# Kernel tuning notes

Hardware: AMD Instinct MI355X
Metric: run time of the kernel (lower is better)

## Reference

```python
import jax, jax.numpy as jnp
import numpy as np

B, S, D, H, HD = 2, 4096, 768, 12, 64
W = 256           # one-sided window (attention_window=512)
C = S // W        # number of query chunks
NEG = -1e9


def _heads(x):
    # [B,S,D] -> [B,H,S,HD]
    return x.reshape(B, S, H, HD).transpose(0, 2, 1, 3)


def setup_inputs() -> dict:
    key = jax.random.key(0)
    ks = jax.random.split(key, 9)
    sc = 0.02
    w = lambda i: jax.random.normal(ks[i], (D, D), jnp.float32) * sc
    return {
        "hidden_states": jax.random.normal(ks[0], (B, S, D), jnp.float32),
        "Wq": w(1), "Wk": w(2), "Wv": w(3),
        "Wqg": w(4), "Wkg": w(5), "Wvg": w(6),
        "Wo": w(7),
        "attention_mask": jnp.ones((B, S), jnp.int32),
    }


def reference(hidden_states, Wq, Wk, Wv, Wqg, Wkg, Wvg, Wo, attention_mask):
    x = hidden_states
    scale = 1.0 / float(np.sqrt(HD))
    q = _heads(x @ Wq) * scale           # [B,H,S,HD]
    k = _heads(x @ Wk)
    v = _heads(x @ Wv)

    # ---- banded sliding-window attention (chunked, no [S,S] matrix) ----
    idx = jnp.arange(C)[:, None] * W + jnp.arange(3 * W)[None, :]   # [C,3W] into padded seq
    key_pos = idx - W                                               # absolute key position
    kp = jnp.pad(k, ((0, 0), (0, 0), (W, W), (0, 0)))
    vp = jnp.pad(v, ((0, 0), (0, 0), (W, W), (0, 0)))
    kc = kp[:, :, idx]                   # [B,H,C,3W,HD]
    vc = vp[:, :, idx]
    qc = q.reshape(B, H, C, W, HD)
    band = jnp.einsum('bhcqd,bhckd->bhcqk', qc, kc)  # [B,H,C,W,3W]

    qi = jnp.arange(W)[:, None]
    kj = jnp.arange(3 * W)[None, :]
    diag_ok = (kj >= qi) & (kj <= qi + 2 * W)              # |i-j| <= W
    valid = (key_pos >= 0) & (key_pos < S) & (key_pos != 0)  # in-range, dedupe global key 0
    mask = diag_ok[None, :, :] & valid[:, None, :]          # [C,W,3W]
    band = jnp.where(mask[None, None], band, NEG)

    # padding mask on keys
    m = jnp.where(attention_mask > 0, 0.0, NEG).astype(jnp.float32)  # [B,S]
    mp = jnp.pad(m, ((0, 0), (W, W)), constant_values=NEG)
    band = band + mp[:, idx][:, None, :, None, :]
    band = band.reshape(B, H, S, 3 * W)

    # every local query also attends to the global (CLS, pos 0) key
    gsc = jnp.einsum('bhsd,bhgd->bhsg', q, k[:, :, 0:1])   # [B,H,S,1]
    gsc = gsc + m[:, 0][:, None, None, None]

    scores = jnp.concatenate([gsc, band], axis=-1)          # [B,H,S,1+3W]
    probs = jax.nn.softmax(scores, axis=-1)
    pg = probs[..., :1]                                     # global-key prob
    pb = probs[..., 1:].reshape(B, H, C, W, 3 * W)
    out = jnp.einsum('bhcqk,bhckd->bhcqd', pb, vc).reshape(B, H, S, HD)
    out = out + pg * v[:, :, 0:1]

    # ---- global query (CLS) full attention with dedicated projections ----
    qg = _heads(x @ Wqg)[:, :, 0:1] * scale                 # [B,H,1,HD]
    kg = _heads(x @ Wkg)
    vg = _heads(x @ Wvg)
    gs = jnp.einsum('bhgd,bhsd->bhgs', qg, kg) + m[:, None, None, :]
    og = jnp.einsum('bhgs,bhsd->bhgd', jax.nn.softmax(gs, axis=-1), vg)
    out = out.at[:, :, 0:1].set(og)

    out = out.transpose(0, 2, 1, 3).reshape(B, S, D) @ Wo
    return out
```

## Files before the change

kernel.cpp:

```cpp
#include <hip/hip_runtime.h>

#define S_LEN 4096
#define NH 12
#define HDIM 64
#define DMODEL 768
#define NEGF -1.0e9f
#define TOK0_SPLITS 16

typedef __attribute__((ext_vector_type(8))) short bf16x8;
typedef __attribute__((ext_vector_type(4))) float f32x4;

__device__ __forceinline__ short f2b(float f) {
  union { float f; unsigned u; } v; v.f = f;
  unsigned r = v.u + 0x7fffu + ((v.u >> 16) & 1u);
  return (short)(r >> 16);
}
__device__ __forceinline__ float b2f(short s) {
  union { unsigned u; float f; } v; v.u = ((unsigned)(unsigned short)s) << 16;
  return v.f;
}

__global__ __launch_bounds__(256) void k_pre(const float* __restrict__ x,
                                             const float* __restrict__ Wq,
                                             const float* __restrict__ Wk,
                                             const float* __restrict__ Wv,
                                             const float* __restrict__ Wkg,
                                             const float* __restrict__ Wvg,
                                             const float* __restrict__ Wo,
                                             const float* __restrict__ Wqg,
                                             const int* __restrict__ amask,
                                             short* __restrict__ xb,
                                             short* __restrict__ W5t,
                                             short* __restrict__ Wot,
                                             float* __restrict__ qg,
                                             float* __restrict__ mvb) {
  __shared__ float smem[1056];
  int bid = blockIdx.x, tid = threadIdx.x;
  if (bid < 6144) {
    int i = bid * 256 + tid;
    float4 v = ((const float4*)x)[i];
    ((short4*)xb)[i] = make_short4(f2b(v.x), f2b(v.y), f2b(v.z), f2b(v.w));
  } else if (bid < 9600) {
    int zb = bid - 6144;
    int z = zb / 576, rem = zb - z * 576;
    int by = rem / 24, bx = rem - by * 24;
    const float* src; float scale = 1.f; short* dst;
    switch (z) {
      case 0: src = Wq;  scale = 0.125f * 1.44269504f; dst = W5t; break;
      case 1: src = Wk;  dst = W5t + 589824; break;
      case 2: src = Wv;  dst = W5t + 2 * 589824; break;
      case 3: src = Wkg; dst = W5t + 3 * 589824; break;
      case 4: src = Wvg; dst = W5t + 4 * 589824; break;
      default: src = Wo; dst = Wot; break;
    }
    int tx = tid & 31, ty = tid >> 5;
    int kb = by * 32, nb = bx * 32;
    for (int i = 0; i < 4; i++) smem[(ty + 8 * i) * 33 + tx] = src[(kb + ty + 8 * i) * 768 + nb + tx];
    __syncthreads();
    for (int i = 0; i < 4; i++)
      dst[(nb + ty + 8 * i) * 768 + kb + tx] = f2b(smem[tx * 33 + ty + 8 * i] * scale);
  } else if (bid < 9632) {
    int zb = bid - 9600;
    int b = zb >> 4, s = (zb & 15) * 256 + tid;
    mvb[b * S_LEN + s] = (s != 0 && amask[b * S_LEN + s] > 0) ? 0.f : NEGF;
  } else {
    int zb = bid - 9632;
    int h = zb % 12, b = zb / 12;
    int out = tid & 63, slice = tid >> 6;
    float* xr = smem;
    float* ps = smem + 768;
    for (int i = tid; i < 768; i += 256) xr[i] = x[(long)b * S_LEN * 768 + i];
    __syncthreads();
    float a = 0.f;
    int n = h * 64 + out;
#pragma unroll 8
    for (int k = slice * 192; k < slice * 192 + 192; k++) a += xr[k] * Wqg[k * 768 + n];
    ps[slice * 64 + out] = a;
    __syncthreads();
    if (tid < 64)
      qg[b * 768 + h * 64 + tid] = (ps[tid] + ps[64 + tid] + ps[128 + tid] + ps[192 + tid]) * 0.125f;
  }
}

__global__ __launch_bounds__(256) void k_gemm(const short* __restrict__ A,
                                              const short* __restrict__ Bt, int K, int mode,
                                              short* __restrict__ qkv, float* __restrict__ outf) {
  __shared__ short Al[2][128 * 32];
  __shared__ short Bl[2][128 * 32];
  int bid = blockIdx.x;
  int xcd = bid & 7, ii = bid >> 3;
  int bm = xcd * 8 + (ii & 7), bn = ii >> 3;
  int tid = threadIdx.x;
  int bm0 = bm * 128, bn0 = bn * 128;
  int w = tid >> 6, lane = tid & 63, g = lane >> 4, r16 = lane & 15;
  int wr = (w >> 1) * 64, wc = (w & 1) * 64;
  f32x4 zero4 = {0.f, 0.f, 0.f, 0.f};
  f32x4 acc[4][4];
  for (int m = 0; m < 4; m++) for (int n = 0; n < 4; n++) acc[m][n] = zero4;
  int srow = w * 32 + (lane >> 2);
  int scol = (lane & 3) * 8;
#define G_STAGE(BUF, KT)                                                              \
  do {                                                                                \
    for (int i = 0; i < 2; i++) {                                                     \
      const short* ga = &A[(long)(bm0 + srow + i * 16) * K + (KT) + scol];            \
      const short* gb = &Bt[(long)(bn0 + srow + i * 16) * K + (KT) + scol];           \
      __builtin_amdgcn_global_load_lds(                                               \
          (const __attribute__((address_space(1))) void*)ga,                          \
          (__attribute__((address_space(3))) void*)&Al[BUF][(w * 32 + i * 16) * 32],  \
          16, 0, 0);                                                                  \
      __builtin_amdgcn_global_load_lds(                                               \
          (const __attribute__((address_space(1))) void*)gb,                          \
          (__attribute__((address_space(3))) void*)&Bl[BUF][(w * 32 + i * 16) * 32],  \
          16, 0, 0);                                                                  \
    }                                                                                 \
  } while (0)
  int nt = K >> 5;
  G_STAGE(0, 0);
  __syncthreads();
  int cur = 0;
  for (int t = 0; t < nt; t++) {
    if (t + 1 < nt) G_STAGE(cur ^ 1, (t + 1) * 32);
    bf16x8 af[4], bfv[4];
    for (int m = 0; m < 4; m++) af[m] = *(const bf16x8*)&Al[cur][(wr + m * 16 + r16) * 32 + g * 8];
    for (int n = 0; n < 4; n++) bfv[n] = *(const bf16x8*)&Bl[cur][(wc + n * 16 + r16) * 32 + g * 8];
    for (int m = 0; m < 4; m++)
      for (int n = 0; n < 4; n++)
        acc[m][n] = __builtin_amdgcn_mfma_f32_16x16x32_bf16(af[m], bfv[n], acc[m][n], 0, 0, 0);
    __syncthreads();
    cur ^= 1;
  }
#undef G_STAGE
  for (int m = 0; m < 4; m++)
    for (int n = 0; n < 4; n++)
      for (int reg = 0; reg < 4; reg++) {
        int row = bm0 + wr + m * 16 + g * 4 + reg;
        int col = bn0 + wc + n * 16 + r16;
        float val = acc[m][n][reg];
        if (mode == 0) {
          int proj = col / 768;
          int rem = col - proj * 768;
          int hh = rem >> 6, d = rem & 63;
          int bb = row >> 12, s = row & 4095;
          qkv[(long)proj * 6291456 + ((((long)bb * NH + hh) * S_LEN + s) << 6) + d] = f2b(val);
        } else {
          outf[(long)row * 768 + col] = val;
        }
      }
}

__global__ __launch_bounds__(256) void k_vt(const short* __restrict__ V, short* __restrict__ Vt) {
  __shared__ short buf[64][72];
  int st = blockIdx.x, bh = blockIdx.y;
  int tid = threadIdx.x;
  long base = (long)bh * S_LEN * HDIM;
  int s0 = st * 64;
  int r = tid >> 2, c = (tid & 3) * 16;
  *(int4*)&buf[r][c]     = *(const int4*)&V[base + (long)(s0 + r) * HDIM + c];
  *(int4*)&buf[r][c + 8] = *(const int4*)&V[base + (long)(s0 + r) * HDIM + c + 8];
  __syncthreads();
  int d = tid >> 2, sc = (tid & 3) * 16;
  short tmp[16];
#pragma unroll
  for (int j = 0; j < 16; j++) tmp[j] = buf[sc + j][d];
  long ob = base + (long)d * S_LEN + s0 + sc;
  *(int4*)&Vt[ob]     = *(const int4*)&tmp[0];
  *(int4*)&Vt[ob + 8] = *(const int4*)&tmp[8];
}

#define PSTRIDE 68

__device__ __forceinline__ void band_chunk(
    int ks0, int qrow0, int g, int r16,
    const bf16x8 (&qf)[2][2], const bf16x8 (&kf)[4][2], const bf16x8 (&vf)[4][2],
    const float (&mv)[4],
    float (&mstate)[2][4], float (&lstate)[2][4], f32x4 (&acc)[2][4],
    short* Plds) {
  int dlo = ks0 - qrow0;
  bool fullok = (dlo >= -224) && (dlo <= 192);
  for (int m = 0; m < 2; m++) {
    f32x4 s[4];
    f32x4 zero4 = {0.f, 0.f, 0.f, 0.f};
    for (int n = 0; n < 4; n++) {
      f32x4 z = __builtin_amdgcn_mfma_f32_16x16x32_bf16(qf[m][0], kf[n][0], zero4, 0, 0, 0);
      s[n] = __builtin_amdgcn_mfma_f32_16x16x32_bf16(qf[m][1], kf[n][1], z, 0, 0, 0);
    }
    float p[4][4], rmax[4];
    for (int reg = 0; reg < 4; reg++) rmax[reg] = NEGF;
    if (fullok) {
      for (int n = 0; n < 4; n++)
        for (int reg = 0; reg < 4; reg++) {
          float val = s[n][reg] + mv[n];
          p[n][reg] = val;
          rmax[reg] = fmaxf(rmax[reg], val);
        }
    } else {
      int qbase = qrow0 + m * 16 + g * 4;
      for (int n = 0; n < 4; n++) {
        int kpos = ks0 + n * 16 + r16;
        for (int reg = 0; reg < 4; reg++) {
          int qpos = qbase + reg;
          bool ok = (kpos >= qpos - 256) && (kpos <= qpos + 256);
          float val = ok ? (s[n][reg] + mv[n]) : NEGF;
          p[n][reg] = val;
          rmax[reg] = fmaxf(rmax[reg], val);
        }
      }
    }
    for (int reg = 0; reg < 4; reg++) {
      float r = rmax[reg];
      r = fmaxf(r, __shfl_xor(r, 1));
      r = fmaxf(r, __shfl_xor(r, 2));
      r = fmaxf(r, __shfl_xor(r, 4));
      r = fmaxf(r, __shfl_xor(r, 8));
      rmax[reg] = r;
    }
    bool over = false;
    for (int reg = 0; reg < 4; reg++) over = over || (rmax[reg] > mstate[m][reg] + 8.f);
    if (__any((int)over)) {
      float scal[4];
      for (int reg = 0; reg < 4; reg++) {
        float mn = fmaxf(mstate[m][reg], rmax[reg]);
        scal[reg] = __builtin_amdgcn_exp2f(mstate[m][reg] - mn);
        mstate[m][reg] = mn;
      }
      float rs[4] = {0.f, 0.f, 0.f, 0.f};
      for (int n = 0; n < 4; n++)
        for (int reg = 0; reg < 4; reg++) {
          float e = __builtin_amdgcn_exp2f(p[n][reg] - mstate[m][reg]);
          p[n][reg] = e;
          rs[reg] += e;
        }
      for (int reg = 0; reg < 4; reg++) {
        float r = rs[reg];
        r += __shfl_xor(r, 1);
        r += __shfl_xor(r, 2);
        r += __shfl_xor(r, 4);
        r += __shfl_xor(r, 8);
        lstate[m][reg] = lstate[m][reg] * scal[reg] + r;
      }
      for (int n = 0; n < 4; n++)
        for (int reg = 0; reg < 4; reg++) acc[m][n][reg] *= scal[reg];
    } else {
      float rs[4] = {0.f, 0.f, 0.f, 0.f};
      for (int n = 0; n < 4; n++)
        for (int reg = 0; reg < 4; reg++) {
          float e = __builtin_amdgcn_exp2f(p[n][reg] - mstate[m][reg]);
          p[n][reg] = e;
          rs[reg] += e;
        }
      for (int reg = 0; reg < 4; reg++) {
        float r = rs[reg];
        r += __shfl_xor(r, 1);
        r += __shfl_xor(r, 2);
        r += __shfl_xor(r, 4);
        r += __shfl_xor(r, 8);
        lstate[m][reg] += r;
      }
    }
    for (int n = 0; n < 4; n++)
      for (int reg = 0; reg < 4; reg++)
        Plds[(g * 4 + reg) * PSTRIDE + n * 16 + r16] = f2b(p[n][reg]);
    bf16x8 pa[2];
    for (int ks = 0; ks < 2; ks++)
      pa[ks] = *(const bf16x8*)&Plds[r16 * PSTRIDE + ks * 32 + g * 8];
    for (int n = 0; n < 4; n++)
      for (int ks = 0; ks < 2; ks++)
        acc[m][n] = __builtin_amdgcn_mfma_f32_16x16x32_bf16(pa[ks], vf[n][ks], acc[m][n], 0, 0, 0);
  }
}

__global__ __launch_bounds__(256, 2) void k_attn(const short* __restrict__ Qb,
                                                 const short* __restrict__ Kb,
                                                 const short* __restrict__ Vb,
                                                 const short* __restrict__ Vtb,
                                                 const short* __restrict__ Kg,
                                                 const short* __restrict__ Vg,
                                                 const float* __restrict__ qg,
                                                 const int* __restrict__ amask,
                                                 const float* __restrict__ mvb,
                                                 short* __restrict__ oattn,
                                                 float* __restrict__ part) {
  __shared__ short Plds[4][16 * PSTRIDE];
  __shared__ float mrg[2][48][65];
  __shared__ float fsm[592];
  int bid = blockIdx.x, tid = threadIdx.x;
  if (bid < 1536) {
    int qt = bid & 63, rest = bid >> 6;
    int h = rest % NH, b = rest / NH;
    int w = tid >> 6, lane = tid & 63, g = lane >> 4, r16 = lane & 15;
    int pair = w >> 1;
    int par = w & 1;
    long bhof = ((long)(b * NH + h)) * S_LEN * HDIM;
    int qrow0 = qt * 64 + pair * 32;

    bf16x8 qf[2][2];
    for (int m = 0; m < 2; m++)
      for (int ks = 0; ks < 2; ks++)
        qf[m][ks] = *(const bf16x8*)&Qb[bhof + (long)(qrow0 + m * 16 + r16) * HDIM + ks * 32 + g * 8];

    float mstate[2][4], lstate[2][4];
    f32x4 acc[2][4];
    if (par == 0) {
      bf16x8 k0f[2];
      for (int ks = 0; ks < 2; ks++) k0f[ks] = *(const bf16x8*)&Kb[bhof + ks * 32 + g * 8];
      float part0[2];
      for (int m = 0; m < 2; m++) {
        float p = 0.f;
        for (int ks = 0; ks < 2; ks++)
          for (int j = 0; j < 8; j++) p += b2f(qf[m][ks][j]) * b2f(k0f[ks][j]);
        p += __shfl_xor(p, 16);
        p += __shfl_xor(p, 32);
        part0[m] = p;
      }
      float mask0 = (amask[b * S_LEN] > 0) ? 0.f : NEGF;
      float v0v[4];
      for (int n = 0; n < 4; n++) v0v[n] = b2f(Vb[bhof + n * 16 + r16]);
      for (int m = 0; m < 2; m++)
        for (int reg = 0; reg < 4; reg++) {
          mstate[m][reg] = __shfl(part0[m], g * 4 + reg) + mask0;
          lstate[m][reg] = 1.f;
          for (int n = 0; n < 4; n++) acc[m][n][reg] = v0v[n];
        }
    } else {
      for (int m = 0; m < 2; m++)
        for (int reg = 0; reg < 4; reg++) {
          mstate[m][reg] = NEGF;
          lstate[m][reg] = 0.f;
          for (int n = 0; n < 4; n++) acc[m][n][reg] = 0.f;
        }
    }

    int wlo = (qrow0 - 256) >> 6; if (wlo < 0) wlo = 0;
    int whi = (qrow0 + 31 + 256) >> 6; if (whi > 63) whi = 63;

    for (int ci = wlo + par; ci <= whi; ci += 2) {
      int ks0 = ci * 64;
      bf16x8 vf[4][2], kf[4][2];
      for (int n = 0; n < 4; n++)
        for (int ks = 0; ks < 2; ks++) {
          vf[n][ks] = *(const bf16x8*)&Vtb[bhof + (long)(n * 16 + r16) * S_LEN + ks0 + ks * 32 + g * 8];
          kf[n][ks] = *(const bf16x8*)&Kb[bhof + (long)(ks0 + n * 16 + r16) * HDIM + ks * 32 + g * 8];
        }
      float mv[4];
      for (int n = 0; n < 4; n++) mv[n] = mvb[b * S_LEN + ks0 + n * 16 + r16];
      band_chunk(ks0, qrow0, g, r16, qf, kf, vf, mv, mstate, lstate, acc, &Plds[w][0]);
    }

    if (par == 1) {
      for (int m = 0; m < 2; m++)
        for (int reg = 0; reg < 4; reg++) {
          mrg[pair][m * 4 + reg][lane] = mstate[m][reg];
          mrg[pair][8 + m * 4 + reg][lane] = lstate[m][reg];
          for (int n = 0; n < 4; n++)
            mrg[pair][16 + m * 16 + n * 4 + reg][lane] = acc[m][n][reg];
        }
    }
    __syncthreads();
    if (par == 0) {
      for (int m = 0; m < 2; m++)
        for (int reg = 0; reg < 4; reg++) {
          float mB = mrg[pair][m * 4 + reg][lane];
          float lB = mrg[pair][8 + m * 4 + reg][lane];
          float M = fmaxf(mstate[m][reg], mB);
          float sA = __builtin_amdgcn_exp2f(mstate[m][reg] - M);
          float sB = __builtin_amdgcn_exp2f(mB - M);
          float l = lstate[m][reg] * sA + lB * sB;
          int token = qrow0 + m * 16 + g * 4 + reg;
          for (int n = 0; n < 4; n++) {
            float a = acc[m][n][reg] * sA + mrg[pair][16 + m * 16 + n * 4 + reg][lane] * sB;
            int col = h * 64 + n * 16 + r16;
            oattn[((long)b * S_LEN + token) * 768 + col] = f2b(a / l);
          }
        }
    }
  } else {
    int tbid = bid - 1536;
    int split = tbid & 15, bhid = tbid >> 4;
    int b = bhid / NH, h = bhid % NH;
    long base = (long)bhid * S_LEN * HDIM;
    int lane = tid & 63, w = tid >> 6;
    int s = split * 256 + tid;
    float* qgl  = fsm;
    float* p_sh = fsm + 64;
    float* red  = fsm + 320;
    float* psum = fsm + 324;
    if (tid < 64) qgl[tid] = qg[b * 768 + h * 64 + tid];
    __syncthreads();
    float dot = 0.f;
    {
      const int4* kr = (const int4*)&Kg[base + (long)s * HDIM];
#pragma unroll
      for (int u = 0; u < 8; u++) {
        int4 pk = kr[u];
        const short* sp = (const short*)&pk;
        for (int j = 0; j < 8; j++) dot += qgl[u * 8 + j] * b2f(sp[j]);
      }
      dot += (amask[b * S_LEN + s] > 0) ? 0.f : NEGF;
    }
    float mx = dot;
    for (int o = 32; o; o >>= 1) mx = fmaxf(mx, __shfl_xor(mx, o));
    if (lane == 0) red[w] = mx;
    __syncthreads();
    mx = fmaxf(fmaxf(red[0], red[1]), fmaxf(red[2], red[3]));
    float e = __expf(dot - mx);
    p_sh[tid] = e;
    float sum = e;
    for (int o = 32; o; o >>= 1) sum += __shfl_xor(sum, o);
    __syncthreads();
    if (lane == 0) red[w] = sum;
    __syncthreads();
    sum = red[0] + red[1] + red[2] + red[3];
    int d = tid & 63, grp = tid >> 6;
    float a = 0.f;
    long vb = base + (long)(split * 256 + grp * 64) * HDIM + d;
#pragma unroll 8
    for (int j = 0; j < 64; j++) a += p_sh[grp * 64 + j] * b2f(Vg[vb + (long)j * HDIM]);
    psum[grp * 64 + d] = a;
    __syncthreads();
    float* dst = &part[((long)bhid * TOK0_SPLITS + split) * 66];
    if (tid == 0) { dst[0] = mx; dst[1] = sum; }
    if (tid < 64)
      dst[2 + tid] = psum[tid] + psum[64 + tid] + psum[128 + tid] + psum[192 + tid];
  }
}

__global__ void k_tok0_comb(const float* __restrict__ part, short* __restrict__ oattn) {
  int bhid = blockIdx.x, d = threadIdx.x;
  int b = bhid / NH, h = bhid % NH;
  const float* p0 = &part[(long)bhid * TOK0_SPLITS * 66];
  float M = NEGF;
  for (int i = 0; i < TOK0_SPLITS; i++) M = fmaxf(M, p0[i * 66]);
  float L = 0.f, a = 0.f;
  for (int i = 0; i < TOK0_SPLITS; i++) {
    float sc = __expf(p0[i * 66] - M);
    L += sc * p0[i * 66 + 1];
    a += sc * p0[i * 66 + 2 + d];
  }
  oattn[((long)b * S_LEN) * 768 + h * 64 + d] = f2b(a / L);
}

extern "C" void kernel_launch(void* const* d_in, const int* in_sizes, int n_in,
                              void* d_out, int out_size, void* d_ws, size_t ws_size,
                              hipStream_t stream) {
  (void)in_sizes; (void)n_in; (void)out_size; (void)ws_size;
  const float* x   = (const float*)d_in[0];
  const float* Wq  = (const float*)d_in[1];
  const float* Wk  = (const float*)d_in[2];
  const float* Wv  = (const float*)d_in[3];
  const float* Wqg = (const float*)d_in[4];
  const float* Wkg = (const float*)d_in[5];
  const float* Wvg = (const float*)d_in[6];
  const float* Wo  = (const float*)d_in[7];
  const int* amask = (const int*)d_in[8];
  char* ws = (char*)d_ws;
  short* xb    = (short*)(ws);
  short* Vt    = (short*)(ws);
  short* W5t   = (short*)(ws + 12582912);
  short* Wot   = (short*)(ws + 18481152);
  short* qkv   = (short*)(ws + 19660800);
  short* oattn = (short*)(ws + 82575360);
  float* qgbuf = (float*)(ws + 95158272);
  float* partb = (float*)(ws + 95164416);
  float* mvb   = (float*)(ws + 95265792);
  float* outf  = (float*)d_out;

  k_pre<<<9656, 256, 0, stream>>>(x, Wq, Wk, Wv, Wkg, Wvg, Wo, Wqg, amask,
                                  xb, W5t, Wot, qgbuf, mvb);
  k_gemm<<<1920, 256, 0, stream>>>(xb, W5t, 768, 0, qkv, nullptr);
  const short* Qb = qkv;
  const short* Kb = qkv + 6291456;
  const short* Vb = qkv + 2 * 6291456;
  const short* Kg = qkv + 3 * 6291456;
  const short* Vg = qkv + 4 * 6291456;
  k_vt<<<dim3(64, 24), 256, 0, stream>>>(Vb, Vt);
  k_attn<<<1920, 256, 0, stream>>>(Qb, Kb, Vb, Vt, Kg, Vg, qgbuf, amask, mvb, oattn, partb);
  k_tok0_comb<<<24, 64, 0, stream>>>(partb, oattn);
  k_gemm<<<384, 256, 0, stream>>>(oattn, Wot, 768, 1, nullptr, outf);
}
```

Before: 200.8 us.

## Split each query tile across four waves and use lazy-max softmax in band attention

Each attention block now handles 32 query rows, with all four waves splitting the key chunks (stride 4) instead of two wave pairs each splitting between two waves. Partial softmax states are combined with a tree merge through shared memory. The per-chunk row-max reduction is dropped: exponentials use the running max directly, and the max is recomputed and rescaled only when a row sum passes a threshold. Shared memory is unified into one buffer so the tok0 path reuses it. This removes shuffle reductions and doubles the number of blocks, at the cost of redundant Q loads, extra barriers and more merge work.

Result: slower. 221.2 us (+10.2%).

```diff
diff --git a/kernel.cpp b/kernel.cpp
--- a/kernel.cpp
+++ b/kernel.cpp
@@ -6,6 +6,7 @@
 #define DMODEL 768
 #define NEGF -1.0e9f
 #define TOK0_SPLITS 16
+#define RSTH 16777216.0f
 
 typedef __attribute__((ext_vector_type(8))) short bf16x8;
 typedef __attribute__((ext_vector_type(4))) float f32x4;
@@ -184,52 +185,66 @@
       f32x4 z = __builtin_amdgcn_mfma_f32_16x16x32_bf16(qf[m][0], kf[n][0], zero4, 0, 0, 0);
       s[n] = __builtin_amdgcn_mfma_f32_16x16x32_bf16(qf[m][1], kf[n][1], z, 0, 0, 0);
     }
-    float p[4][4], rmax[4];
-    for (int reg = 0; reg < 4; reg++) rmax[reg] = NEGF;
+    float p[4][4];
+    float rs[4] = {0.f, 0.f, 0.f, 0.f};
+    int qbase = qrow0 + m * 16 + g * 4;
     if (fullok) {
       for (int n = 0; n < 4; n++)
         for (int reg = 0; reg < 4; reg++) {
-          float val = s[n][reg] + mv[n];
-          p[n][reg] = val;
-          rmax[reg] = fmaxf(rmax[reg], val);
+          float e = __builtin_amdgcn_exp2f(s[n][reg] + mv[n] - mstate[m][reg]);
+          p[n][reg] = e;
+          rs[reg] += e;
         }
     } else {
-      int qbase = qrow0 + m * 16 + g * 4;
       for (int n = 0; n < 4; n++) {
         int kpos = ks0 + n * 16 + r16;
         for (int reg = 0; reg < 4; reg++) {
           int qpos = qbase + reg;
           bool ok = (kpos >= qpos - 256) && (kpos <= qpos + 256);
+          float e = ok ? __builtin_amdgcn_exp2f(s[n][reg] + mv[n] - mstate[m][reg]) : 0.f;
+          p[n][reg] = e;
+          rs[reg] += e;
+        }
+      }
+    }
+    bool ovf = (rs[0] > RSTH) || (rs[1] > RSTH) || (rs[2] > RSTH) || (rs[3] > RSTH);
+    if (__any((int)ovf)) {
+      float rmax[4];
+      for (int reg = 0; reg < 4; reg++) rmax[reg] = NEGF;
+      for (int n = 0; n < 4; n++) {
+        int kpos = ks0 + n * 16 + r16;
+        for (int reg = 0; reg < 4; reg++) {
+          int qpos = qbase + reg;
+          bool ok = fullok || ((kpos >= qpos - 256) && (kpos <= qpos + 256));
           float val = ok ? (s[n][reg] + mv[n]) : NEGF;
-          p[n][reg] = val;
           rmax[reg] = fmaxf(rmax[reg], val);
         }
       }
-    }
-    for (int reg = 0; reg < 4; reg++) {
-      float r = rmax[reg];
-      r = fmaxf(r, __shfl_xor(r, 1));
-      r = fmaxf(r, __shfl_xor(r, 2));
-      r = fmaxf(r, __shfl_xor(r, 4));
-      r = fmaxf(r, __shfl_xor(r, 8));
-      rmax[reg] = r;
-    }
-    bool over = false;
-    for (int reg = 0; reg < 4; reg++) over = over || (rmax[reg] > mstate[m][reg] + 8.f);
-    if (__any((int)over)) {
+      for (int reg = 0; reg < 4; reg++) {
+        float r = rmax[reg];
+        r = fmaxf(r, __shfl_xor(r, 1));
+        r = fmaxf(r, __shfl_xor(r, 2));
+        r = fmaxf(r, __shfl_xor(r, 4));
+        r = fmaxf(r, __shfl_xor(r, 8));
+        rmax[reg] = r;
+      }
       float scal[4];
       for (int reg = 0; reg < 4; reg++) {
         float mn = fmaxf(mstate[m][reg], rmax[reg]);
         scal[reg] = __builtin_amdgcn_exp2f(mstate[m][reg] - mn);
         mstate[m][reg] = mn;
-      }
-      float rs[4] = {0.f, 0.f, 0.f, 0.f};
-      for (int n = 0; n < 4; n++)
-        for (int reg = 0; reg < 4; reg++) {
-          float e = __builtin_amdgcn_exp2f(p[n][reg] - mstate[m][reg]);
+        rs[reg] = 0.f;
+      }
+      for (int n = 0; n < 4; n++) {
+        int kpos = ks0 + n * 16 + r16;
+        for (int reg = 0; reg < 4; reg++) {
+          int qpos = qbase + reg;
+          bool ok = fullok || ((kpos >= qpos - 256) && (kpos <= qpos + 256));
+          float e = ok ? __builtin_amdgcn_exp2f(s[n][reg] + mv[n] - mstate[m][reg]) : 0.f;
           p[n][reg] = e;
           rs[reg] += e;
         }
+      }
       for (int reg = 0; reg < 4; reg++) {
         float r = rs[reg];
         r += __shfl_xor(r, 1);
@@ -241,13 +256,6 @@
       for (int n = 0; n < 4; n++)
         for (int reg = 0; reg < 4; reg++) acc[m][n][reg] *= scal[reg];
     } else {
-      float rs[4] = {0.f, 0.f, 0.f, 0.f};
-      for (int n = 0; n < 4; n++)
-        for (int reg = 0; reg < 4; reg++) {
-          float e = __builtin_amdgcn_exp2f(p[n][reg] - mstate[m][reg]);
-          p[n][reg] = e;
-          rs[reg] += e;
-        }
       for (int reg = 0; reg < 4; reg++) {
         float r = rs[reg];
         r += __shfl_xor(r, 1);
@@ -280,18 +288,16 @@
                                                  const float* __restrict__ mvb,
                                                  short* __restrict__ oattn,
                                                  float* __restrict__ part) {
-  __shared__ short Plds[4][16 * PSTRIDE];
-  __shared__ float mrg[2][48][65];
-  __shared__ float fsm[592];
+  __shared__ __align__(16) char shbuf[24960];
   int bid = blockIdx.x, tid = threadIdx.x;
-  if (bid < 1536) {
-    int qt = bid & 63, rest = bid >> 6;
+  if (bid < 3072) {
+    int qt = bid & 127, rest = bid >> 7;
     int h = rest % NH, b = rest / NH;
     int w = tid >> 6, lane = tid & 63, g = lane >> 4, r16 = lane & 15;
-    int pair = w >> 1;
-    int par = w & 1;
     long bhof = ((long)(b * NH + h)) * S_LEN * HDIM;
-    int qrow0 = qt * 64 + pair * 32;
+    int qrow0 = qt * 32;
+    short* PldsW = (short*)shbuf + w * (16 * PSTRIDE);
+    float (*mrg)[48][65] = (float (*)[48][65])shbuf;
 
     bf16x8 qf[2][2];
     for (int m = 0; m < 2; m++)
@@ -300,7 +306,7 @@
 
     float mstate[2][4], lstate[2][4];
     f32x4 acc[2][4];
-    if (par == 0) {
+    if (w == 0) {
       bf16x8 k0f[2];
       for (int ks = 0; ks < 2; ks++) k0f[ks] = *(const bf16x8*)&Kb[bhof + ks * 32 + g * 8];
       float part0[2];
@@ -317,14 +323,17 @@
       for (int n = 0; n < 4; n++) v0v[n] = b2f(Vb[bhof + n * 16 + r16]);
       for (int m = 0; m < 2; m++)
         for (int reg = 0; reg < 4; reg++) {
-          mstate[m][reg] = __shfl(part0[m], g * 4 + reg) + mask0;
-          lstate[m][reg] = 1.f;
-          for (int n = 0; n < 4; n++) acc[m][n][reg] = v0v[n];
+          float m0raw = __shfl(part0[m], g * 4 + reg) + mask0;
+          float m0 = fmaxf(m0raw, -60.f);
+          mstate[m][reg] = m0;
+          float l0 = __builtin_amdgcn_exp2f(m0raw - m0);
+          lstate[m][reg] = l0;
+          for (int n = 0; n < 4; n++) acc[m][n][reg] = l0 * v0v[n];
         }
     } else {
       for (int m = 0; m < 2; m++)
         for (int reg = 0; reg < 4; reg++) {
-          mstate[m][reg] = NEGF;
+          mstate[m][reg] = 0.f;
           lstate[m][reg] = 0.f;
           for (int n = 0; n < 4; n++) acc[m][n][reg] = 0.f;
         }
@@ -333,7 +342,7 @@
     int wlo = (qrow0 - 256) >> 6; if (wlo < 0) wlo = 0;
     int whi = (qrow0 + 31 + 256) >> 6; if (whi > 63) whi = 63;
 
-    for (int ci = wlo + par; ci <= whi; ci += 2) {
+    for (int ci = wlo + w; ci <= whi; ci += 4) {
       int ks0 = ci * 64;
       bf16x8 vf[4][2], kf[4][2];
       for (int n = 0; n < 4; n++)
@@ -343,43 +352,63 @@
         }
       float mv[4];
       for (int n = 0; n < 4; n++) mv[n] = mvb[b * S_LEN + ks0 + n * 16 + r16];
-      band_chunk(ks0, qrow0, g, r16, qf, kf, vf, mv, mstate, lstate, acc, &Plds[w][0]);
-    }
-
-    if (par == 1) {
+      band_chunk(ks0, qrow0, g, r16, qf, kf, vf, mv, mstate, lstate, acc, PldsW);
+    }
+
+#define WRITE_STATE(SLOT)                                                  \
+    for (int m = 0; m < 2; m++)                                            \
+      for (int reg = 0; reg < 4; reg++) {                                  \
+        mrg[SLOT][m * 4 + reg][lane] = mstate[m][reg];                     \
+        mrg[SLOT][8 + m * 4 + reg][lane] = lstate[m][reg];                 \
+        for (int n = 0; n < 4; n++)                                        \
+          mrg[SLOT][16 + m * 16 + n * 4 + reg][lane] = acc[m][n][reg];     \
+      }
+#define MERGE_FROM(SLOT)                                                   \
+    for (int m = 0; m < 2; m++)                                            \
+      for (int reg = 0; reg < 4; reg++) {                                  \
+        float mB = mrg[SLOT][m * 4 + reg][lane];                           \
+        float lB = mrg[SLOT][8 + m * 4 + reg][lane];                       \
+        float M = fmaxf(mstate[m][reg], mB);                               \
+        float sA = __builtin_amdgcn_exp2f(mstate[m][reg] - M);             \
+        float sB = __builtin_amdgcn_exp2f(mB - M);                         \
+        mstate[m][reg] = M;                                                \
+        lstate[m][reg] = lstate[m][reg] * sA + lB * sB;                    \
+        for (int n = 0; n < 4; n++)                                        \
+          acc[m][n][reg] = acc[m][n][reg] * sA +                           \
+                           mrg[SLOT][16 + m * 16 + n * 4 + reg][lane] * sB;\
+      }
+
+    __syncthreads();
+    if (w == 1) { WRITE_STATE(0) }
+    if (w == 3) { WRITE_STATE(1) }
+    __syncthreads();
+    if (w == 0) { MERGE_FROM(0) }
+    if (w == 2) { MERGE_FROM(1) }
+    __syncthreads();
+    if (w == 2) { WRITE_STATE(0) }
+    __syncthreads();
+    if (w == 0) {
+      MERGE_FROM(0)
       for (int m = 0; m < 2; m++)
         for (int reg = 0; reg < 4; reg++) {
-          mrg[pair][m * 4 + reg][lane] = mstate[m][reg];
-          mrg[pair][8 + m * 4 + reg][lane] = lstate[m][reg];
-          for (int n = 0; n < 4; n++)
-            mrg[pair][16 + m * 16 + n * 4 + reg][lane] = acc[m][n][reg];
-        }
-    }
-    __syncthreads();
-    if (par == 0) {
-      for (int m = 0; m < 2; m++)
-        for (int reg = 0; reg < 4; reg++) {
-          float mB = mrg[pair][m * 4 + reg][lane];
-          float lB = mrg[pair][8 + m * 4 + reg][lane];
-          float M = fmaxf(mstate[m][reg], mB);
-          float sA = __builtin_amdgcn_exp2f(mstate[m][reg] - M);
-          float sB = __builtin_amdgcn_exp2f(mB - M);
-          float l = lstate[m][reg] * sA + lB * sB;
           int token = qrow0 + m * 16 + g * 4 + reg;
           for (int n = 0; n < 4; n++) {
-            float a = acc[m][n][reg] * sA + mrg[pair][16 + m * 16 + n * 4 + reg][lane] * sB;
             int col = h * 64 + n * 16 + r16;
-            oattn[((long)b * S_LEN + token) * 768 + col] = f2b(a / l);
+            oattn[((long)b * S_LEN + token) * 768 + col] =
+                f2b(acc[m][n][reg] / lstate[m][reg]);
           }
         }
     }
+#undef WRITE_STATE
+#undef MERGE_FROM
   } else {
-    int tbid = bid - 1536;
+    int tbid = bid - 3072;
     int split = tbid & 15, bhid = tbid >> 4;
     int b = bhid / NH, h = bhid % NH;
     long base = (long)bhid * S_LEN * HDIM;
     int lane = tid & 63, w = tid >> 6;
     int s = split * 256 + tid;
+    float* fsm  = (float*)shbuf;
     float* qgl  = fsm;
     float* p_sh = fsm + 64;
     float* red  = fsm + 320;
@@ -473,7 +502,7 @@
   const short* Kg = qkv + 3 * 6291456;
   const short* Vg = qkv + 4 * 6291456;
   k_vt<<<dim3(64, 24), 256, 0, stream>>>(Vb, Vt);
-  k_attn<<<1920, 256, 0, stream>>>(Qb, Kb, Vb, Vt, Kg, Vg, qgbuf, amask, mvb, oattn, partb);
+  k_attn<<<3456, 256, 0, stream>>>(Qb, Kb, Vb, Vt, Kg, Vg, qgbuf, amask, mvb, oattn, partb);
   k_tok0_comb<<<24, 64, 0, stream>>>(partb, oattn);
   k_gemm<<<384, 256, 0, stream>>>(oattn, Wot, 768, 1, nullptr, outf);
 }
```
